# Performance work log

Measured on AMD Instinct MI355X. Metric: run time of the kernel, lower is better.

Reference implementation:

```python
import jax, jax.numpy as jnp
import numpy as np

N, E = 50000, 800000
IN, HID, OUT, H = 128, 32, 32, 4
NEG_SLOPE = 0.2
EPS = 1e-5


def layernorm(x, g, b):
    mu = x.mean(-1, keepdims=True)
    var = ((x - mu) ** 2).mean(-1, keepdims=True)
    return (x - mu) * jax.lax.rsqrt(var + EPS) * g + b


def gat_conv(x, src, dst, W, a_s, a_d, bias, heads, ch, concat):
    n = x.shape[0]
    h = (x @ W).reshape(n, heads, ch)               # [N,H,C]
    alpha_s = (h * a_s).sum(-1)                     # [N,H]
    alpha_d = (h * a_d).sum(-1)                     # [N,H]
    e = jax.nn.leaky_relu(alpha_s[src] + alpha_d[dst], NEG_SLOPE)  # [E,H]
    m = jax.ops.segment_max(e, dst, num_segments=n)
    m = jnp.where(jnp.isfinite(m), m, 0.0)
    ex = jnp.exp(e - m[dst])
    denom = jax.ops.segment_sum(ex, dst, num_segments=n)
    alpha = ex / (denom[dst] + 1e-16)               # [E,H]
    msg = h[src] * alpha[:, :, None]                # [E,H,C]
    out = jax.ops.segment_sum(msg, dst, num_segments=n)  # [N,H,C]
    out = out.reshape(n, heads * ch) if concat else out.mean(axis=1)
    return out + bias


def setup_inputs() -> dict:
    key = jax.random.key(0)
    ks = jax.random.split(key, 24)
    HC = HID * H
    s = 0.05
    inp = {
        "x": jax.random.normal(ks[0], (N, IN), jnp.float32),
        "edge_index": jax.random.randint(ks[1], (2, E), 0, N),
        "W1": jax.random.normal(ks[2], (IN, HC), jnp.float32) * s,
        "as1": jax.random.normal(ks[3], (H, HID), jnp.float32) * s,
        "ad1": jax.random.normal(ks[4], (H, HID), jnp.float32) * s,
        "b1": jnp.zeros((HC,), jnp.float32),
        "g1": jnp.ones((HC,), jnp.float32),
        "be1": jnp.zeros((HC,), jnp.float32),
        "W2": jax.random.normal(ks[5], (HC, HC), jnp.float32) * s,
        "as2": jax.random.normal(ks[6], (H, HID), jnp.float32) * s,
        "ad2": jax.random.normal(ks[7], (H, HID), jnp.float32) * s,
        "b2": jnp.zeros((HC,), jnp.float32),
        "g2": jnp.ones((HC,), jnp.float32),
        "be2": jnp.zeros((HC,), jnp.float32),
        "W3": jax.random.normal(ks[8], (HC, OUT * H), jnp.float32) * s,
        "as3": jax.random.normal(ks[9], (H, OUT), jnp.float32) * s,
        "ad3": jax.random.normal(ks[10], (H, OUT), jnp.float32) * s,
        "b3": jnp.zeros((OUT,), jnp.float32),
        "Wsk": jax.random.normal(ks[11], (IN, HC), jnp.float32) * s,
        "bsk": jnp.zeros((HC,), jnp.float32),
    }
    return inp


def reference(x, edge_index, W1, as1, ad1, b1, g1, be1, W2, as2, ad2, b2, g2, be2, W3, as3, ad3, b3, Wsk, bsk):
    n = x.shape[0]
    loops = jnp.arange(n, dtype=edge_index.dtype)
    src = jnp.concatenate([edge_index[0], loops])
    dst = jnp.concatenate([edge_index[1], loops])
    h = gat_conv(x, src, dst, W1, as1, ad1, b1, H, HID, True)
    h = jax.nn.elu(h)
    h = layernorm(h, g1, be1)
    h = h + (x @ Wsk + bsk)  # residual (dropout is identity in eval)
    h = gat_conv(h, src, dst, W2, as2, ad2, b2, H, HID, True)
    h = jax.nn.elu(h)
    h = layernorm(h, g2, be2)
    h = gat_conv(h, src, dst, W3, as3, ad3, b3, H, OUT, False)
    return h
```

## Files before the change

kernel.cpp:

```cpp
#include <hip/hip_runtime.h>
#include <hip/hip_bf16.h>

typedef __attribute__((ext_vector_type(8))) short short8;
typedef __attribute__((ext_vector_type(4))) float f32x4;
using bf16 = __hip_bfloat16;

#define NEG_SLOPE 0.2f
#define LN_EPS 1e-5f
#define SCAT_EPB 8192

__device__ __forceinline__ unsigned short f2bfu(float v) {
    bf16 t = __float2bfloat16(v);
    unsigned short s;
    __builtin_memcpy(&s, &t, 2);
    return s;
}
__device__ __forceinline__ short f2bf(float v) {
    bf16 t = __float2bfloat16(v);
    short s;
    __builtin_memcpy(&s, &t, 2);
    return s;
}
__device__ __forceinline__ unsigned packbf(float a, float b) {
    return (unsigned)f2bfu(a) | ((unsigned)f2bfu(b) << 16);
}
__device__ __forceinline__ float bflo(unsigned u) { return __uint_as_float(u << 16); }
__device__ __forceinline__ float bfhi(unsigned u) { return __uint_as_float(u & 0xffff0000u); }

__device__ __forceinline__ int computeFlag(const void* x) {
    const uint4* u4 = (const uint4*)x;
    int lane = threadIdx.x & 63;
    float m = 0.f;
    for (int i = lane; i < 1024; i += 64) {
        uint4 q = u4[i];
        unsigned vv[4] = {q.x, q.y, q.z, q.w};
#pragma unroll
        for (int k = 0; k < 4; ++k) {
            float a = fabsf(bflo(vv[k]));
            float b = fabsf(bfhi(vv[k]));
            m = fmaxf(m, (a == a) ? a : 1e30f);
            m = fmaxf(m, (b == b) ? b : 1e30f);
        }
    }
    for (int d = 1; d < 64; d <<= 1) m = fmaxf(m, __shfl_xor(m, d));
    return (m > 1e4f) ? 1 : 0;
}

struct Ptr4 { const void* p[4]; };
struct Ptr14 { const void* p[14]; };
struct Ptr3 { const void* p[3]; };
struct Ptr6 { const void* p[6]; };
__global__ void stage_k(const void* __restrict__ x,
                        Ptr4 Ws, bf16* __restrict__ WT,
                        Ptr14 ptrs, bf16* __restrict__ sv,
                        Ptr3 Wv, Ptr6 av, bf16* __restrict__ vaT,
                        int* __restrict__ dtFlag, int* __restrict__ bucketCur,
                        int CAP) {
    int b = blockIdx.x;
    int f = computeFlag(x);
    if (b < 256) {
        int gid = b * 256 + threadIdx.x;
        int m = gid >> 14;
        int idx = gid & 16383;
        int i = idx >> 7, j = idx & 127;
        const void* W = Ws.p[m];
        float v = f ? ((const float*)W)[idx]
                    : __bfloat162float(((const bf16*)W)[idx]);
        WT[m * 16384 + j * 128 + i] = __float2bfloat16(v);
    } else if (b == 256) {
        for (int i = threadIdx.x; i < 512; i += 256) bucketCur[i] = i * CAP;
        if (threadIdx.x == 0) dtFlag[0] = f;
        for (int k = threadIdx.x; k < 14 * 128; k += 256) {
            int t = k >> 7, i = k & 127;
            int n = (t == 12) ? 32 : 128;
            if (i < n) {
                const void* s = ptrs.p[t];
                float v = f ? ((const float*)s)[i]
                            : __bfloat162float(((const bf16*)s)[i]);
                sv[k] = __float2bfloat16(v);
            }
        }
    } else {
        int gid = (b - 257) * 256 + threadIdx.x;
        int l = gid >> 11;
        if (l >= 3) return;
        int c = (gid >> 7) & 15, k = gid & 127;
        float acc = 0.f;
        if (c < 8) {
            int hd = c & 3;
            const void* W = Wv.p[l];
            const void* a = av.p[l * 2 + (c >> 2)];
            for (int j = 0; j < 32; ++j) {
                float wv = f ? ((const float*)W)[k * 128 + hd * 32 + j]
                             : __bfloat162float(((const bf16*)W)[k * 128 + hd * 32 + j]);
                float avv = f ? ((const float*)a)[hd * 32 + j]
                              : __bfloat162float(((const bf16*)a)[hd * 32 + j]);
                acc += wv * avv;
            }
        }
        vaT[gid] = __float2bfloat16(acc);
    }
}

__global__ __launch_bounds__(256) void mega1_k(
        const void* __restrict__ A, const bf16* __restrict__ WT,
        bf16* __restrict__ out0, bf16* __restrict__ out1,
        const bf16* __restrict__ bias1, const bf16* __restrict__ vaT,
        float* __restrict__ asN, float* __restrict__ adN,
        int N, const int* __restrict__ flag, int scatB, int gb,
        const int* __restrict__ src, const int* __restrict__ dst,
        int* bucketCur, int* __restrict__ ebuf, int E, int NB, int CAP) {
    __shared__ int lcnt[512], lbase[512];
    if ((int)blockIdx.x < scatB) {
        int t = threadIdx.x;
        int e0 = (int)blockIdx.x * SCAT_EPB;
        int cnt = E - e0;
        if (cnt > SCAT_EPB) cnt = SCAT_EPB;
        for (int i = t; i < NB; i += 256) lcnt[i] = 0;
        __syncthreads();
        for (int i = t; i < cnt; i += 256)
            atomicAdd(&lcnt[dst[e0 + i] >> 7], 1);
        __syncthreads();
        for (int i = t; i < NB; i += 256) {
            int c = lcnt[i];
            lbase[i] = c ? atomicAdd(&bucketCur[i], c) : 0;
            lcnt[i] = 0;
        }
        __syncthreads();
        for (int i = t; i < cnt; i += 256) {
            int d = dst[e0 + i];
            int b = d >> 7;
            int pos = lbase[b] + atomicAdd(&lcnt[b], 1);
            if (pos < (b + 1) * CAP)
                ebuf[pos] = ((d & 127) << 16) | src[e0 + i];
        }
        return;
    }
    int wave = threadIdx.x >> 6, lane = threadIdx.x & 63;
    int lm = lane & 15, lk = lane >> 4;
    const short* Ws = (const short*)WT;
    const short* Vs = (const short*)vaT;
    bool f32m = flag[0] != 0;

    short8 bw0[2][4], bw1[2][4];
#pragma unroll
    for (int ct = 0; ct < 2; ++ct) {
        int c = (wave * 2 + ct) * 16 + lm;
#pragma unroll
        for (int kk = 0; kk < 4; ++kk) {
            bw0[ct][kk] = *(const short8*)(Ws + (size_t)c * 128 + kk * 32 + lk * 8);
            bw1[ct][kk] = *(const short8*)(Ws + 16384 + (size_t)c * 128 + kk * 32 + lk * 8);
        }
    }
    short8 va8[4];
    if (wave == 0) {
#pragma unroll
        for (int kk = 0; kk < 4; ++kk)
            va8[kk] = *(const short8*)(Vs + (size_t)lm * 128 + kk * 32 + lk * 8);
    }
    float bv[2][4];
#pragma unroll
    for (int ct = 0; ct < 2; ++ct) {
        int c0 = (wave * 2 + ct) * 16 + lk * 4;
#pragma unroll
        for (int i = 0; i < 4; ++i)
            bv[ct][i] = __bfloat162float(bias1[c0 + i]);
    }

    int stride = gb * 32;
    for (int rowBase = ((int)blockIdx.x - scatB) * 32; rowBase < N; rowBase += stride) {
        short8 af[2][4];
#pragma unroll
        for (int rt = 0; rt < 2; ++rt) {
            int r = rowBase + rt * 16 + lm;
            if (r >= N) r = N - 1;
            if (f32m) {
#pragma unroll
                for (int kk = 0; kk < 4; ++kk) {
                    const float* Af = (const float*)A + (size_t)r * 128 + kk * 32 + lk * 8;
                    float4 q0 = *(const float4*)(Af);
                    float4 q1 = *(const float4*)(Af + 4);
                    short8 v;
                    v[0] = f2bf(q0.x); v[1] = f2bf(q0.y); v[2] = f2bf(q0.z); v[3] = f2bf(q0.w);
                    v[4] = f2bf(q1.x); v[5] = f2bf(q1.y); v[6] = f2bf(q1.z); v[7] = f2bf(q1.w);
                    af[rt][kk] = v;
                }
            } else {
#pragma unroll
                for (int kk = 0; kk < 4; ++kk)
                    af[rt][kk] = *(const short8*)((const short*)A + (size_t)r * 128 + kk * 32 + lk * 8);
            }
        }

        f32x4 acc0[2][2], acc1[2][2];
#pragma unroll
        for (int ct = 0; ct < 2; ++ct)
#pragma unroll
            for (int rt = 0; rt < 2; ++rt) {
                acc0[ct][rt] = (f32x4){0.f, 0.f, 0.f, 0.f};
                acc1[ct][rt] = (f32x4){0.f, 0.f, 0.f, 0.f};
            }
#pragma unroll
        for (int rt = 0; rt < 2; ++rt) {
#pragma unroll
            for (int kk = 0; kk < 4; ++kk) {
                acc0[0][rt] = __builtin_amdgcn_mfma_f32_16x16x32_bf16(bw0[0][kk], af[rt][kk], acc0[0][rt], 0, 0, 0);
                acc0[1][rt] = __builtin_amdgcn_mfma_f32_16x16x32_bf16(bw0[1][kk], af[rt][kk], acc0[1][rt], 0, 0, 0);
                acc1[0][rt] = __builtin_amdgcn_mfma_f32_16x16x32_bf16(bw1[0][kk], af[rt][kk], acc1[0][rt], 0, 0, 0);
                acc1[1][rt] = __builtin_amdgcn_mfma_f32_16x16x32_bf16(bw1[1][kk], af[rt][kk], acc1[1][rt], 0, 0, 0);
            }
        }
#pragma unroll
        for (int ct = 0; ct < 2; ++ct) {
            int c0 = (wave * 2 + ct) * 16 + lk * 4;
#pragma unroll
            for (int rt = 0; rt < 2; ++rt) {
                int r = rowBase + rt * 16 + lm;
                if (r < N) {
                    uint2 pk0, pk1;
                    pk0.x = packbf(acc0[ct][rt][0], acc0[ct][rt][1]);
                    pk0.y = packbf(acc0[ct][rt][2], acc0[ct][rt][3]);
                    pk1.x = packbf(acc1[ct][rt][0] + bv[ct][0], acc1[ct][rt][1] + bv[ct][1]);
                    pk1.y = packbf(acc1[ct][rt][2] + bv[ct][2], acc1[ct][rt][3] + bv[ct][3]);
                    *(uint2*)((unsigned short*)out0 + (size_t)r * 128 + c0) = pk0;
                    *(uint2*)((unsigned short*)out1 + (size_t)r * 128 + c0) = pk1;
                }
            }
        }
        if (wave == 0) {
            f32x4 accA[2];
#pragma unroll
            for (int rt = 0; rt < 2; ++rt) accA[rt] = (f32x4){0.f, 0.f, 0.f, 0.f};
#pragma unroll
            for (int rt = 0; rt < 2; ++rt)
#pragma unroll
                for (int kk = 0; kk < 4; ++kk)
                    accA[rt] = __builtin_amdgcn_mfma_f32_16x16x32_bf16(va8[kk], af[rt][kk], accA[rt], 0, 0, 0);
            if (lk < 2) {
                float* dp = lk ? adN : asN;
#pragma unroll
                for (int rt = 0; rt < 2; ++rt) {
                    int r = rowBase + rt * 16 + lm;
                    if (r < N) *(f32x4*)(dp + (size_t)r * 4) = accA[rt];
                }
            }
        }
    }
}

__global__ __launch_bounds__(256) void build_k(const int* __restrict__ ebuf,
                                               const int* __restrict__ bucketCur,
                                               int* __restrict__ rowSE,
                                               int* __restrict__ colSrc,
                                               int N, int CAP) {
    int b = blockIdx.x, t = threadIdx.x;
    int base = b * CAP;
    int cnt = bucketCur[b] - base;
    if (cnt > CAP) cnt = CAP;
    __shared__ int nodeCnt[128], nodeCur[128], ws2[2];
    if (t < 128) nodeCnt[t] = 0;
    __syncthreads();
    for (int i = t; i < cnt; i += 256)
        atomicAdd(&nodeCnt[ebuf[base + i] >> 16], 1);
    __syncthreads();
    int v = 0, incl = 0;
    if (t < 128) {
        v = nodeCnt[t];
        incl = v;
        for (int d = 1; d < 64; d <<= 1) {
            int u = __shfl_up(incl, d);
            if ((t & 63) >= d) incl += u;
        }
        if ((t & 63) == 63) ws2[t >> 6] = incl;
    }
    __syncthreads();
    if (t < 128) {
        int excl = incl - v + ((t >= 64) ? ws2[0] : 0);
        int node = b * 128 + t;
        if (node < N) {
            rowSE[node * 2] = base + excl;
            rowSE[node * 2 + 1] = base + excl + v;
        }
        nodeCur[t] = excl;
    }
    __syncthreads();
    for (int i = t; i < cnt; i += 256) {
        int p = ebuf[base + i];
        int pos = base + atomicAdd(&nodeCur[p >> 16], 1);
        colSrc[pos] = (p & 0xffff) << 8;
    }
}

__global__ __launch_bounds__(256) void gemm_k(const void* __restrict__ A,
                                              const bf16* __restrict__ WT,
                                              bf16* __restrict__ out0,
                                              const bf16* __restrict__ vaT,
                                              float* __restrict__ asN,
                                              float* __restrict__ adN,
                                              int N) {
    int wave = threadIdx.x >> 6, lane = threadIdx.x & 63;
    int lm = lane & 15, lk = lane >> 4;
    const short* Ws = (const short*)WT;
    const short* Vs = (const short*)vaT;

    short8 bw0[2][4];
#pragma unroll
    for (int ct = 0; ct < 2; ++ct) {
        int c = (wave * 2 + ct) * 16 + lm;
#pragma unroll
        for (int kk = 0; kk < 4; ++kk)
            bw0[ct][kk] = *(const short8*)(Ws + (size_t)c * 128 + kk * 32 + lk * 8);
    }
    short8 va8[4];
    if (wave == 0) {
#pragma unroll
        for (int kk = 0; kk < 4; ++kk)
            va8[kk] = *(const short8*)(Vs + (size_t)lm * 128 + kk * 32 + lk * 8);
    }

    int stride = gridDim.x * 32;
    for (int rowBase = blockIdx.x * 32; rowBase < N; rowBase += stride) {
        short8 af[2][4];
#pragma unroll
        for (int rt = 0; rt < 2; ++rt) {
            int r = rowBase + rt * 16 + lm;
            if (r >= N) r = N - 1;
#pragma unroll
            for (int kk = 0; kk < 4; ++kk)
                af[rt][kk] = *(const short8*)((const short*)A + (size_t)r * 128 + kk * 32 + lk * 8);
        }

        f32x4 acc0[2][2];
#pragma unroll
        for (int ct = 0; ct < 2; ++ct)
#pragma unroll
            for (int rt = 0; rt < 2; ++rt) acc0[ct][rt] = (f32x4){0.f, 0.f, 0.f, 0.f};
#pragma unroll
        for (int rt = 0; rt < 2; ++rt) {
#pragma unroll
            for (int kk = 0; kk < 4; ++kk) {
                acc0[0][rt] = __builtin_amdgcn_mfma_f32_16x16x32_bf16(bw0[0][kk], af[rt][kk], acc0[0][rt], 0, 0, 0);
                acc0[1][rt] = __builtin_amdgcn_mfma_f32_16x16x32_bf16(bw0[1][kk], af[rt][kk], acc0[1][rt], 0, 0, 0);
            }
        }
#pragma unroll
        for (int ct = 0; ct < 2; ++ct) {
            int c0 = (wave * 2 + ct) * 16 + lk * 4;
#pragma unroll
            for (int rt = 0; rt < 2; ++rt) {
                int r = rowBase + rt * 16 + lm;
                if (r < N) {
                    uint2 pk;
                    pk.x = packbf(acc0[ct][rt][0], acc0[ct][rt][1]);
                    pk.y = packbf(acc0[ct][rt][2], acc0[ct][rt][3]);
                    *(uint2*)((unsigned short*)out0 + (size_t)r * 128 + c0) = pk;
                }
            }
        }
        if (wave == 0) {
            f32x4 accA[2];
#pragma unroll
            for (int rt = 0; rt < 2; ++rt) accA[rt] = (f32x4){0.f, 0.f, 0.f, 0.f};
#pragma unroll
            for (int rt = 0; rt < 2; ++rt)
#pragma unroll
                for (int kk = 0; kk < 4; ++kk)
                    accA[rt] = __builtin_amdgcn_mfma_f32_16x16x32_bf16(va8[kk], af[rt][kk], accA[rt], 0, 0, 0);
            if (lk < 2) {
                float* dp = lk ? adN : asN;
#pragma unroll
                for (int rt = 0; rt < 2; ++rt) {
                    int r = rowBase + rt * 16 + lm;
                    if (r < N) *(f32x4*)(dp + (size_t)r * 4) = accA[rt];
                }
            }
        }
    }
}

template <int MODE>
__global__ __launch_bounds__(256) void agg_k(const bf16* __restrict__ h,
                                             const float* __restrict__ asN,
                                             const float* __restrict__ adN,
                                             const int* __restrict__ rowSE,
                                             const int* __restrict__ colSrc,
                                             const bf16* __restrict__ bvec,
                                             const bf16* __restrict__ g,
                                             const bf16* __restrict__ be,
                                             void* outv, int N,
                                             const int* __restrict__ flag) {
    int wv = threadIdx.x >> 6, lane = threadIdx.x & 63;
    int grp = lane >> 4, t = lane & 15;
    int hd = t >> 2;
    const char* hbase = (const char*)h + t * 16;
    const char* abase = (const char*)asN + hd * 4;
    int f = (MODE == 3 && flag) ? flag[0] : 0;
    int nstride = gridDim.x * 4;

    for (int n = blockIdx.x * 4 + wv; n < N; n += nstride) {
        int2 se = ((const int2*)rowSE)[n];
        int st = se.x, en = se.y;
        if (en < st) en = st;

        float adn = adN[(size_t)n * 4 + hd];
        float asn_self = asN[(size_t)n * 4 + hd];
        unsigned hs = *(const unsigned*)((const char*)h + (size_t)n * 256 + t * 16 + grp * 4);

        float a[8];
#pragma unroll
        for (int k = 0; k < 8; ++k) a[k] = 0.f;
        float den = 0.f;

        int j = st + grp;
        int o0 = (j      < en) ? colSrc[j]      : 0;
        int o1 = (j + 4  < en) ? colSrc[j + 4]  : 0;
        int o2 = (j + 8  < en) ? colSrc[j + 8]  : 0;
        int o3 = (j + 12 < en) ? colSrc[j + 12] : 0;
        float av0 = *(const float*)(abase + (o0 >> 4));
        uint4 hq0 = *(const uint4*)(hbase + o0);
        float av1 = *(const float*)(abase + (o1 >> 4));
        uint4 hq1 = *(const uint4*)(hbase + o1);
        float av2 = *(const float*)(abase + (o2 >> 4));
        uint4 hq2 = *(const uint4*)(hbase + o2);
        for (; j < en; j += 4) {
            int o4 = (j + 16 < en) ? colSrc[j + 16] : 0;
            float av3 = *(const float*)(abase + (o3 >> 4));
            uint4 hq3 = *(const uint4*)(hbase + o3);
            float e = av0 + adn;
            float w = __expf(fmaxf(e, NEG_SLOPE * e));
            den += w;
            a[0] += w * bflo(hq0.x); a[1] += w * bfhi(hq0.x);
            a[2] += w * bflo(hq0.y); a[3] += w * bfhi(hq0.y);
            a[4] += w * bflo(hq0.z); a[5] += w * bfhi(hq0.z);
            a[6] += w * bflo(hq0.w); a[7] += w * bfhi(hq0.w);
            o3 = o4;
            av0 = av1; hq0 = hq1;
            av1 = av2; hq1 = hq2;
            av2 = av3; hq2 = hq3;
        }

#pragma unroll
        for (int k = 0; k < 8; ++k) {
            a[k] += __shfl_xor(a[k], 16);
            a[k] += __shfl_xor(a[k], 32);
        }
        den += __shfl_xor(den, 16);
        den += __shfl_xor(den, 32);

        float es = asn_self + adn;
        float wsf = __expf(fmaxf(es, NEG_SLOPE * es));
        den += wsf;

        float s0 = (grp & 1) ? a[2] : a[0];
        float s1 = (grp & 1) ? a[3] : a[1];
        float s2 = (grp & 1) ? a[6] : a[4];
        float s3 = (grp & 1) ? a[7] : a[5];
        float p0 = (grp & 2) ? s2 : s0;
        float p1 = (grp & 2) ? s3 : s1;

        p0 += wsf * bflo(hs);
        p1 += wsf * bfhi(hs);

        float inv = 1.f / (den + 1e-16f);
        float y0 = p0 * inv, y1 = p1 * inv;

        if (MODE == 3) {
            y0 += __shfl_xor(y0, 4); y0 += __shfl_xor(y0, 8); y0 *= 0.25f;
            y1 += __shfl_xor(y1, 4); y1 += __shfl_xor(y1, 8); y1 *= 0.25f;
            if (t < 4) {
                int oc = t * 8 + grp * 2;
                unsigned bp = *(const unsigned*)((const char*)bvec + oc * 2);
                float v0 = y0 + bflo(bp), v1 = y1 + bfhi(bp);
                if (f) {
                    *(float2*)((float*)outv + (size_t)n * 32 + oc) = make_float2(v0, v1);
                } else {
                    ((unsigned*)outv)[(size_t)n * 16 + (oc >> 1)] = packbf(v0, v1);
                }
            }
        } else {
            unsigned short* out = (unsigned short*)outv;
            int boff = t * 16 + grp * 4;
            unsigned bp = *(const unsigned*)((const char*)bvec + boff);
            y0 += bflo(bp); y1 += bfhi(bp);
            y0 = y0 > 0.f ? y0 : (__expf(y0) - 1.f);
            y1 = y1 > 0.f ? y1 : (__expf(y1) - 1.f);
            float s = y0 + y1, q = y0 * y0 + y1 * y1;
#pragma unroll
            for (int d = 1; d < 64; d <<= 1) {
                s += __shfl_xor(s, d);
                q += __shfl_xor(q, d);
            }
            float mu = s * (1.f / 128.f);
            float var = q * (1.f / 128.f) - mu * mu;
            var = fmaxf(var, 0.f);
            float rs = rsqrtf(var + LN_EPS);
            unsigned gp = *(const unsigned*)((const char*)g + boff);
            unsigned ep = *(const unsigned*)((const char*)be + boff);
            float z0 = (y0 - mu) * rs * bflo(gp) + bflo(ep);
            float z1 = (y1 - mu) * rs * bfhi(gp) + bfhi(ep);
            char* op = (char*)out + (size_t)n * 256 + boff;
            if (MODE == 1) {
                unsigned sk = *(const unsigned*)op;
                z0 += bflo(sk); z1 += bfhi(sk);
            }
            *(unsigned*)op = packbf(z0, z1);
        }
    }
}

extern "C" void kernel_launch(void* const* d_in, const int* in_sizes, int n_in,
                              void* d_out, int out_size, void* d_ws, size_t ws_size,
                              hipStream_t stream) {
    const void* x  = d_in[0];
    const int*  ei = (const int*)d_in[1];

    int N = in_sizes[0] / 128;
    int E = in_sizes[1] / 2;
    const int* srcI = ei;
    const int* dstI = ei + E;

    int NB = (N + 127) >> 7;
    int CAP = (E / NB + 1024 + 511) & ~511;

    char* w = (char*)d_ws;
    size_t o = 0;
    auto carve = [&](size_t bytes) {
        void* p = w + o;
        o += (bytes + 255) & ~(size_t)255;
        return p;
    };
    int*  dtFlag = (int*)carve(256);
    bf16* WTall = (bf16*)carve(4 * 16384 * 2);
    bf16* sv   = (bf16*)carve(14 * 128 * 2);
    bf16* vaT  = (bf16*)carve(3 * 16 * 128 * 2);
    bf16* hB   = (bf16*)carve((size_t)N * 128 * 2);
    bf16* xB   = (bf16*)carve((size_t)N * 128 * 2);
    float* asN = (float*)carve((size_t)N * 4 * 4);
    float* adN = (float*)carve((size_t)N * 4 * 4);
    int* rowSE = (int*)carve((size_t)N * 2 * 4);
    int* colSrc= (int*)carve((size_t)NB * CAP * 4 + 128);
    int* ebuf  = (int*)carve((size_t)NB * CAP * 4);
    int* bucketCur = (int*)carve(512 * 4);

    Ptr4 wp;
    wp.p[0] = d_in[2];  wp.p[1] = d_in[18];
    wp.p[2] = d_in[8];  wp.p[3] = d_in[14];
    Ptr14 ptrs;
    ptrs.p[0] = d_in[3];  ptrs.p[1] = d_in[4];  ptrs.p[2] = d_in[5];
    ptrs.p[3] = d_in[6];  ptrs.p[4] = d_in[7];
    ptrs.p[5] = d_in[9];  ptrs.p[6] = d_in[10]; ptrs.p[7] = d_in[11];
    ptrs.p[8] = d_in[12]; ptrs.p[9] = d_in[13];
    ptrs.p[10] = d_in[15]; ptrs.p[11] = d_in[16]; ptrs.p[12] = d_in[17];
    ptrs.p[13] = d_in[19];
    Ptr3 wv3;
    wv3.p[0] = d_in[2]; wv3.p[1] = d_in[8]; wv3.p[2] = d_in[14];
    Ptr6 av6;
    av6.p[0] = d_in[3];  av6.p[1] = d_in[4];
    av6.p[2] = d_in[9];  av6.p[3] = d_in[10];
    av6.p[4] = d_in[15]; av6.p[5] = d_in[16];

    stage_k<<<281, 256, 0, stream>>>(x, wp, WTall, ptrs, sv, wv3, av6, vaT,
                                     dtFlag, bucketCur, CAP);

    int gb = (N + 63) / 64;
    int scatB = (E + SCAT_EPB - 1) / SCAT_EPB;
    int nQuads = (N + 3) / 4;
    int aggGrid = nQuads < 2048 ? nQuads : 2048;

    mega1_k<<<scatB + gb, 256, 0, stream>>>(x, WTall, hB, xB, sv + 13 * 128,
                                            vaT, asN, adN, N, dtFlag, scatB, gb,
                                            srcI, dstI, bucketCur, ebuf, E, NB, CAP);

    build_k<<<NB, 256, 0, stream>>>(ebuf, bucketCur, rowSE, colSrc, N, CAP);

    agg_k<1><<<aggGrid, 256, 0, stream>>>(hB, asN, adN, rowSE, colSrc,
                                          sv + 2 * 128, sv + 3 * 128, sv + 4 * 128,
                                          xB, N, dtFlag);

    gemm_k<<<gb, 256, 0, stream>>>(xB, WTall + 2 * 16384, hB,
                                   vaT + 2048, asN, adN, N);
    agg_k<2><<<aggGrid, 256, 0, stream>>>(hB, asN, adN, rowSE, colSrc,
                                          sv + 7 * 128, sv + 8 * 128, sv + 9 * 128,
                                          xB, N, dtFlag);

    gemm_k<<<gb, 256, 0, stream>>>(xB, WTall + 3 * 16384, hB,
                                   vaT + 4096, asN, adN, N);
    agg_k<3><<<aggGrid, 256, 0, stream>>>(hB, asN, adN, rowSE, colSrc,
                                          sv + 12 * 128, nullptr, nullptr,
                                          d_out, N, dtFlag);
}
```

Before: 306.4 us.

## Replace bucketed CSR build with degree count, single-block scan, and atomic scatter

Replaces the two-level bucket sort (per-block shared histograms into 128-node buckets, then a per-bucket local sort) with a global per-node degree count done in the first fused kernel, a single-block exclusive scan over all node degrees, and a per-edge atomic scatter into a compact CSR array. This drops the intermediate edge buffer and the padded bucket capacity, and the degree array is zeroed inside the staging kernel. The cost is one more launch, a serial single-block scan over 50k nodes, and global atomics on hot per-node counters. Edge order within each row is no longer deterministic.

```diff
diff --git a/kernel.cpp b/kernel.cpp
--- a/kernel.cpp
+++ b/kernel.cpp
@@ -7,7 +7,7 @@
 
 #define NEG_SLOPE 0.2f
 #define LN_EPS 1e-5f
-#define SCAT_EPB 8192
+#define SCT_EPB 8192
 
 __device__ __forceinline__ unsigned short f2bfu(float v) {
     bf16 t = __float2bfloat16(v);
@@ -54,8 +54,8 @@
                         Ptr4 Ws, bf16* __restrict__ WT,
                         Ptr14 ptrs, bf16* __restrict__ sv,
                         Ptr3 Wv, Ptr6 av, bf16* __restrict__ vaT,
-                        int* __restrict__ dtFlag, int* __restrict__ bucketCur,
-                        int CAP) {
+                        int* __restrict__ dtFlag,
+                        int* __restrict__ deg, int NZ) {
     int b = blockIdx.x;
     int f = computeFlag(x);
     if (b < 256) {
@@ -67,8 +67,11 @@
         float v = f ? ((const float*)W)[idx]
                     : __bfloat162float(((const bf16*)W)[idx]);
         WT[m * 16384 + j * 128 + i] = __float2bfloat16(v);
+        int zc = (NZ + 255) >> 8;
+        int z0 = b * zc, z1 = z0 + zc;
+        if (z1 > NZ) z1 = NZ;
+        for (int z = z0 + threadIdx.x; z < z1; z += 256) deg[z] = 0;
     } else if (b == 256) {
-        for (int i = threadIdx.x; i < 512; i += 256) bucketCur[i] = i * CAP;
         if (threadIdx.x == 0) dtFlag[0] = f;
         for (int k = threadIdx.x; k < 14 * 128; k += 256) {
             int t = k >> 7, i = k & 127;
@@ -107,33 +110,14 @@
         bf16* __restrict__ out0, bf16* __restrict__ out1,
         const bf16* __restrict__ bias1, const bf16* __restrict__ vaT,
         float* __restrict__ asN, float* __restrict__ adN,
-        int N, const int* __restrict__ flag, int scatB, int gb,
-        const int* __restrict__ src, const int* __restrict__ dst,
-        int* bucketCur, int* __restrict__ ebuf, int E, int NB, int CAP) {
-    __shared__ int lcnt[512], lbase[512];
-    if ((int)blockIdx.x < scatB) {
-        int t = threadIdx.x;
-        int e0 = (int)blockIdx.x * SCAT_EPB;
+        int N, const int* __restrict__ flag, int cntB, int gb,
+        const int* __restrict__ dst, int* __restrict__ deg, int E) {
+    if ((int)blockIdx.x < cntB) {
+        int e0 = (int)blockIdx.x * SCT_EPB;
         int cnt = E - e0;
-        if (cnt > SCAT_EPB) cnt = SCAT_EPB;
-        for (int i = t; i < NB; i += 256) lcnt[i] = 0;
-        __syncthreads();
-        for (int i = t; i < cnt; i += 256)
-            atomicAdd(&lcnt[dst[e0 + i] >> 7], 1);
-        __syncthreads();
-        for (int i = t; i < NB; i += 256) {
-            int c = lcnt[i];
-            lbase[i] = c ? atomicAdd(&bucketCur[i], c) : 0;
-            lcnt[i] = 0;
-        }
-        __syncthreads();
-        for (int i = t; i < cnt; i += 256) {
-            int d = dst[e0 + i];
-            int b = d >> 7;
-            int pos = lbase[b] + atomicAdd(&lcnt[b], 1);
-            if (pos < (b + 1) * CAP)
-                ebuf[pos] = ((d & 127) << 16) | src[e0 + i];
-        }
+        if (cnt > SCT_EPB) cnt = SCT_EPB;
+        for (int i = threadIdx.x; i < cnt; i += 256)
+            atomicAdd(&deg[dst[e0 + i]], 1);
         return;
     }
     int wave = threadIdx.x >> 6, lane = threadIdx.x & 63;
@@ -168,7 +152,7 @@
     }
 
     int stride = gb * 32;
-    for (int rowBase = ((int)blockIdx.x - scatB) * 32; rowBase < N; rowBase += stride) {
+    for (int rowBase = ((int)blockIdx.x - cntB) * 32; rowBase < N; rowBase += stride) {
         short8 af[2][4];
 #pragma unroll
         for (int rt = 0; rt < 2; ++rt) {
@@ -248,46 +232,62 @@
     }
 }
 
-__global__ __launch_bounds__(256) void build_k(const int* __restrict__ ebuf,
-                                               const int* __restrict__ bucketCur,
-                                               int* __restrict__ rowSE,
-                                               int* __restrict__ colSrc,
-                                               int N, int CAP) {
-    int b = blockIdx.x, t = threadIdx.x;
-    int base = b * CAP;
-    int cnt = bucketCur[b] - base;
-    if (cnt > CAP) cnt = CAP;
-    __shared__ int nodeCnt[128], nodeCur[128], ws2[2];
-    if (t < 128) nodeCnt[t] = 0;
+__global__ __launch_bounds__(256) void scan_k(const int* __restrict__ deg,
+                                              int* __restrict__ rowSE,
+                                              int* __restrict__ colCur,
+                                              int N) {
+    __shared__ int wsum[4];
+    int t = threadIdx.x;
+    int nvec = (N + 3) >> 2;
+    int per = (nvec + 255) >> 8;
+    int v0 = t * per, v1 = v0 + per;
+    if (v1 > nvec) v1 = nvec;
+    const int4* d4 = (const int4*)deg;
+    int s = 0;
+    for (int i = v0; i < v1; ++i) {
+        int4 q = d4[i];
+        s += q.x + q.y + q.z + q.w;
+    }
+    int incl = s;
+    for (int d = 1; d < 64; d <<= 1) {
+        int u = __shfl_up(incl, d);
+        if ((t & 63) >= d) incl += u;
+    }
+    if ((t & 63) == 63) wsum[t >> 6] = incl;
     __syncthreads();
-    for (int i = t; i < cnt; i += 256)
-        atomicAdd(&nodeCnt[ebuf[base + i] >> 16], 1);
-    __syncthreads();
-    int v = 0, incl = 0;
-    if (t < 128) {
-        v = nodeCnt[t];
-        incl = v;
-        for (int d = 1; d < 64; d <<= 1) {
-            int u = __shfl_up(incl, d);
-            if ((t & 63) >= d) incl += u;
-        }
-        if ((t & 63) == 63) ws2[t >> 6] = incl;
-    }
-    __syncthreads();
-    if (t < 128) {
-        int excl = incl - v + ((t >= 64) ? ws2[0] : 0);
-        int node = b * 128 + t;
-        if (node < N) {
-            rowSE[node * 2] = base + excl;
-            rowSE[node * 2 + 1] = base + excl + v;
-        }
-        nodeCur[t] = excl;
-    }
-    __syncthreads();
-    for (int i = t; i < cnt; i += 256) {
-        int p = ebuf[base + i];
-        int pos = base + atomicAdd(&nodeCur[p >> 16], 1);
-        colSrc[pos] = (p & 0xffff) << 8;
+    int w = t >> 6, woff = 0;
+#pragma unroll
+    for (int k = 0; k < 3; ++k) if (k < w) woff += wsum[k];
+    int cum = incl - s + woff;
+    for (int i = v0; i < v1; ++i) {
+        int4 q = d4[i];
+        int dd[4] = {q.x, q.y, q.z, q.w};
+        int n0 = i * 4;
+#pragma unroll
+        for (int k = 0; k < 4; ++k) {
+            int n = n0 + k;
+            if (n < N) {
+                rowSE[n * 2] = cum;
+                rowSE[n * 2 + 1] = cum + dd[k];
+                colCur[n] = cum;
+                cum += dd[k];
+            }
+        }
+    }
+}
+
+__global__ __launch_bounds__(256) void scatter_k(const int* __restrict__ src,
+                                                 const int* __restrict__ dst,
+                                                 int* colCur,
+                                                 int* __restrict__ colSrc,
+                                                 int E) {
+    int e0 = blockIdx.x * SCT_EPB;
+    int cnt = E - e0;
+    if (cnt > SCT_EPB) cnt = SCT_EPB;
+    for (int i = threadIdx.x; i < cnt; i += 256) {
+        int d = dst[e0 + i];
+        int pos = atomicAdd(&colCur[d], 1);
+        colSrc[pos] = src[e0 + i] << 8;
     }
 }
 
@@ -519,8 +519,7 @@
     const int* srcI = ei;
     const int* dstI = ei + E;
 
-    int NB = (N + 127) >> 7;
-    int CAP = (E / NB + 1024 + 511) & ~511;
+    int NZ = (N + 7) & ~7;
 
     char* w = (char*)d_ws;
     size_t o = 0;
@@ -538,9 +537,9 @@
     float* asN = (float*)carve((size_t)N * 4 * 4);
     float* adN = (float*)carve((size_t)N * 4 * 4);
     int* rowSE = (int*)carve((size_t)N * 2 * 4);
-    int* colSrc= (int*)carve((size_t)NB * CAP * 4 + 128);
-    int* ebuf  = (int*)carve((size_t)NB * CAP * 4);
-    int* bucketCur = (int*)carve(512 * 4);
+    int* colSrc= (int*)carve((size_t)E * 4 + 128);
+    int* deg   = (int*)carve((size_t)NZ * 4);
+    int* colCur= (int*)carve((size_t)N * 4);
 
     Ptr4 wp;
     wp.p[0] = d_in[2];  wp.p[1] = d_in[18];
@@ -560,18 +559,20 @@
     av6.p[4] = d_in[15]; av6.p[5] = d_in[16];
 
     stage_k<<<281, 256, 0, stream>>>(x, wp, WTall, ptrs, sv, wv3, av6, vaT,
-                                     dtFlag, bucketCur, CAP);
+                                     dtFlag, deg, NZ);
 
     int gb = (N + 63) / 64;
-    int scatB = (E + SCAT_EPB - 1) / SCAT_EPB;
+    int cntB = (E + SCT_EPB - 1) / SCT_EPB;
     int nQuads = (N + 3) / 4;
     int aggGrid = nQuads < 2048 ? nQuads : 2048;
 
-    mega1_k<<<scatB + gb, 256, 0, stream>>>(x, WTall, hB, xB, sv + 13 * 128,
-                                            vaT, asN, adN, N, dtFlag, scatB, gb,
-                                            srcI, dstI, bucketCur, ebuf, E, NB, CAP);
-
-    build_k<<<NB, 256, 0, stream>>>(ebuf, bucketCur, rowSE, colSrc, N, CAP);
+    mega1_k<<<cntB + gb, 256, 0, stream>>>(x, WTall, hB, xB, sv + 13 * 128,
+                                           vaT, asN, adN, N, dtFlag, cntB, gb,
+                                           dstI, deg, E);
+
+    scan_k<<<1, 256, 0, stream>>>(deg, rowSE, colCur, N);
+
+    scatter_k<<<cntB, 256, 0, stream>>>(srcI, dstI, colCur, colSrc, E);
 
     agg_k<1><<<aggGrid, 256, 0, stream>>>(hB, asN, adN, rowSE, colSrc,
                                           sv + 2 * 128, sv + 3 * 128, sv + 4 * 128,
```

New measurement: 421.6 us. 1.38x slower.
